# Kernel tuning notes

Hardware: AMD Instinct MI355X
Metric: run time of the kernel (lower is better)

## Reference

```python
import jax, jax.numpy as jnp
import numpy as np

B, N, D_PATCH = 32, 196, 768
TKN, QK, H, HID = 768, 64, 12, 3072
K_STEPS = 12
ALPHA = 1.0
BETA = 1.0 / (QK ** 0.5)
EPS = 1e-5


def setup_inputs() -> dict:
    key = jax.random.key(0)
    ks = jax.random.split(key, 8)
    w_std = 0.002
    return {
        "x": jax.random.normal(ks[0], (B, N, D_PATCH), jnp.float32),
        "w_enc": jax.random.normal(ks[1], (TKN, D_PATCH), jnp.float32) * 0.02,
        "b_enc": jnp.zeros((TKN,), jnp.float32),
        "cls_tok": jnp.ones((1, 1, TKN), jnp.float32),
        "pos": jax.random.normal(ks[2], (1, N + 1, TKN), jnp.float32) * w_std,
        "eln_gamma": jnp.ones((1,), jnp.float32),
        "eln_bias": jnp.zeros((TKN,), jnp.float32),
        "wq": jax.random.normal(ks[3], (H, QK, TKN), jnp.float32) * w_std,
        "wk": jax.random.normal(ks[4], (H, QK, TKN), jnp.float32) * w_std,
        "w_hop": jax.random.normal(ks[5], (HID, TKN), jnp.float32) * 0.02,
        "dec_ln_w": jnp.ones((TKN,), jnp.float32),
        "dec_ln_b": jnp.zeros((TKN,), jnp.float32),
        "w_dec": jax.random.normal(ks[6], (D_PATCH, TKN), jnp.float32) * 0.02,
        "b_dec": jnp.zeros((D_PATCH,), jnp.float32),
    }


def _energy(g, wq, wk, w_hop):
    # attention energy: non-softmax, -1/beta * sum logsumexp(beta * A)
    q = jnp.einsum('bnd,hzd->bnhz', g, wq)
    k = jnp.einsum('bnd,hzd->bnhz', g, wk)
    A = jnp.einsum('bqhz,bkhz->bhqk', q, k)  # [B,H,N+1,N+1]
    e_attn = (-1.0 / BETA) * jnp.sum(jax.nn.logsumexp(BETA * A, axis=-1))
    # Hopfield energy: -0.5 * sum relu(g W^T)^2
    h = jnp.einsum('bnd,fd->bnf', g, w_hop)  # [B,N+1,HID]
    e_hop = -0.5 * jnp.sum(jax.nn.relu(h) ** 2)
    return e_attn + e_hop


def _energy_ln(x, gamma, bias):
    xm = x - x.mean(-1, keepdims=True)
    o = xm / jnp.sqrt((xm ** 2).mean(-1, keepdims=True) + EPS)
    return gamma * o + bias


def _layernorm(x, w, b):
    mu = x.mean(-1, keepdims=True)
    xm = x - mu
    var = (xm ** 2).mean(-1, keepdims=True)
    return xm / jnp.sqrt(var + EPS) * w + b


def reference(x, w_enc, b_enc, cls_tok, pos, eln_gamma, eln_bias,
              wq, wk, w_hop, dec_ln_w, dec_ln_b, w_dec, b_dec):
    # encode: Linear(d_patch -> tkn)
    t = jnp.einsum('bnd,td->bnt', x, w_enc) + b_enc
    # prepend cls, add positional encoding
    cls = jnp.broadcast_to(cls_tok, (t.shape[0], 1, TKN))
    t = jnp.concatenate([cls, t], axis=1) + pos  # [B, N+1, TKN]

    grad_e = jax.grad(lambda g: _energy(g, wq, wk, w_hop))
    for _ in range(K_STEPS):  # fixed unroll over time steps (single block)
        g = _energy_ln(t, eln_gamma, eln_bias)
        t = t - ALPHA * grad_e(g)

    # decode: LayerNorm + Linear(tkn -> d_patch)
    y = _layernorm(t, dec_ln_w, dec_ln_b)
    y = jnp.einsum('bnt,dt->bnd', y, w_dec) + b_dec
    return y[:, 1:]  # drop cls token (use_cls=False)
```

## Files before the change

### kernel.cpp

```cpp
#include <hip/hip_runtime.h>
#include <hip/hip_bf16.h>

typedef __hip_bfloat16 bf16;
typedef short s8 __attribute__((ext_vector_type(8)));
typedef short sv4 __attribute__((ext_vector_type(4)));
typedef float f4 __attribute__((ext_vector_type(4)));

#define BETA 0.125f
#define EPS 1e-5f

__device__ __forceinline__ void gld16(const void* g, void* l){
    __builtin_amdgcn_global_load_lds(
        (const __attribute__((address_space(1))) void*)g,
        (__attribute__((address_space(3))) void*)l, 16, 0, 0);
}

__global__ __launch_bounds__(256) void f2b_k(const float* __restrict__ in, bf16* __restrict__ out, long n){
    long i = (long)blockIdx.x*256 + threadIdx.x;
    if (i < n) out[i] = __float2bfloat16(in[i]);
}
__global__ __launch_bounds__(256) void padx_k(const float* __restrict__ x, bf16* __restrict__ xb){
    long i = (long)blockIdx.x*256 + threadIdx.x;
    if (i >= 6400L*768) return;
    long row = i / 768;
    xb[i] = (row < 6272) ? __float2bfloat16(x[i]) : __float2bfloat16(0.f);
}
__global__ __launch_bounds__(256) void tr_k(const short* __restrict__ Bi, short* __restrict__ Bo){
    __shared__ short t[32][33];
    int i0 = blockIdx.x*32, j0 = blockIdx.y*32;
    int li = threadIdx.x & 31, lj = threadIdx.x >> 5;
    #pragma unroll
    for (int r=0;r<4;r++) t[lj+8*r][li] = Bi[(long)(i0+lj+8*r)*768 + j0+li];
    __syncthreads();
    #pragma unroll
    for (int r=0;r<4;r++) Bo[(long)(j0+lj+8*r)*4608 + i0+li] = t[li][lj+8*r];
}

__global__ __launch_bounds__(256) void cls_k(const float* __restrict__ cls, const float* __restrict__ pos,
                                             float* __restrict__ t){
    int i = blockIdx.x*256 + threadIdx.x;
    int b = i / 768, c = i % 768;
    t[((long)b*197)*768 + c] = cls[c] + pos[c];
}

template<int MODE>
__global__ __launch_bounds__(256) void big_gemm(
    const short* __restrict__ A, int lda,
    const short* __restrict__ B, int ldb,
    float* __restrict__ Cf, bf16* __restrict__ Cb, int ldc,
    int K, int Nn, int Nm, int relu0, long zoff,
    const float* __restrict__ bias, const float* __restrict__ pos)
{
    const int f = blockIdx.x;
    const int npg = 16*Nn;
    const int grp = f / npg;
    const int first_m = grp*16;
    const int gs = (Nm - first_m < 16) ? (Nm - first_m) : 16;
    const int rem = f % npg;
    const int bm = first_m + rem % gs;
    const int bn = rem / gs;

    __shared__ short lsA[8192];
    __shared__ short lsB[8192];
    const int tid = threadIdx.x;
    const int w = tid>>6, l = tid&63;
    const int m0 = bm*128, n0 = bn*128;
    const int srow = tid>>2;
    const int qglob = ((tid&3) - (tid>>3)) & 3;
    const int scol = qglob*8;
    int koff, Ks;
    if (MODE==1){ Ks = K>>1; koff = blockIdx.z * Ks; Cf += (size_t)blockIdx.z * zoff; }
    else        { Ks = K;    koff = 0; }
    const short* pa = A + (size_t)(m0+srow)*lda + koff + scol;
    const short* pb = B + (size_t)(n0+srow)*ldb + koff + scol;
    short* laP = lsA + w*512;
    short* lbP = lsB + w*512;
    const int wm = (w>>1)*64, wn = (w&1)*64;
    const int fr = l&15, fq = ((l>>4) + (fr>>1) & 3)*8;
    f4 acc[4][4] = {};
    const int nk = Ks>>6;
    for (int kt=0; kt<nk; kt++){
        const size_t ko = (size_t)kt*64;
        const size_t ra = 64*(size_t)lda, rb = 64*(size_t)ldb;
        gld16(pa + ko,           laP);
        gld16(pa + ko + ra,      laP + 2048);
        gld16(pa + ko + 32,      laP + 4096);
        gld16(pa + ko + 32 + ra, laP + 6144);
        gld16(pb + ko,           lbP);
        gld16(pb + ko + rb,      lbP + 2048);
        gld16(pb + ko + 32,      lbP + 4096);
        gld16(pb + ko + 32 + rb, lbP + 6144);
        __syncthreads();
        #pragma unroll
        for (int ks=0; ks<2; ks++){
            s8 af[4], bfr[4];
            #pragma unroll
            for (int i=0;i<4;i++) af[i]  = *(const s8*)(lsA + ks*4096 + (wm+i*16+fr)*32 + fq);
            #pragma unroll
            for (int j=0;j<4;j++) bfr[j] = *(const s8*)(lsB + ks*4096 + (wn+j*16+fr)*32 + fq);
            #pragma unroll
            for (int i=0;i<4;i++)
                #pragma unroll
                for (int j=0;j<4;j++)
                    acc[i][j] = __builtin_amdgcn_mfma_f32_16x16x32_bf16(af[i], bfr[j], acc[i][j], 0,0,0);
        }
        __syncthreads();
    }
    const int er = (l>>4)*4;
    const int ec = l&15;
    #pragma unroll
    for (int i=0;i<4;i++){
        #pragma unroll
        for (int j=0;j<4;j++){
            int gr0 = m0 + wm + i*16 + er;
            int gc  = n0 + wn + j*16 + ec;
            #pragma unroll
            for (int r=0;r<4;r++){
                float v = acc[i][j][r];
                int gr = gr0 + r;
                if (MODE==0){
                    if (gc >= relu0) v = v>0.f ? v : 0.f;
                    Cb[(size_t)gr*ldc + gc] = __float2bfloat16(v);
                } else if (MODE==1){
                    Cf[(size_t)gr*ldc + gc] = v;
                } else if (MODE==2){
                    if (gr < 6272){
                        int b = gr/196, n = gr%196;
                        Cf[((size_t)b*197 + n + 1)*768 + gc] = v + bias[gc] + pos[(long)(n+1)*768+gc];
                    }
                } else {
                    if (gr < 6272) Cf[(size_t)gr*ldc + gc] = v + bias[gc];
                }
            }
        }
    }
}

template<int MODE>
__global__ __launch_bounds__(256, 2) void wide_gemm(
    const short* __restrict__ A, int lda,
    const short* __restrict__ B, int ldb,
    float* __restrict__ Cf, float* __restrict__ Cf2,
    bf16* __restrict__ Cb, int ldc,
    int K, int Nn, int Nm, int relu0, long zoff)
{
    const int f = blockIdx.x;
    const int npg = 16*Nn;
    const int grp = f / npg;
    const int first_m = grp*16;
    const int gs = (Nm - first_m < 16) ? (Nm - first_m) : 16;
    const int rem = f % npg;
    const int bm = first_m + rem % gs;
    const int bn = rem / gs;

    __shared__ short lsA[16384];
    __shared__ short lsB[8192];
    const int tid = threadIdx.x;
    const int w = tid>>6, l = tid&63;
    const int m0 = bm*256, n0 = bn*128;

    int Ks, koff; float* Cp = Cf;
    if (MODE==1){ Ks = K/3; koff = blockIdx.z * Ks;
                  Cp = (blockIdx.z==2) ? Cf2 : Cf + (size_t)blockIdx.z * zoff; }
    else        { Ks = K; koff = 0; }
    const int NT = Ks>>6;

    const short* sA[4]; const short* sB[2];
    #pragma unroll
    for (int j=0;j<4;j++){
        int c = j*256 + tid;
        int r = (c>>2)&255, qd = c&3;
        int qs = (qd - (r>>1)) & 3;
        sA[j] = A + (size_t)(m0+r)*lda + koff + qs*8;
    }
    #pragma unroll
    for (int j=0;j<2;j++){
        int c = j*256 + tid;
        int r = (c>>2)&127, qd = c&3;
        int qs = (qd - (r>>1)) & 3;
        sB[j] = B + (size_t)(n0+r)*ldb + koff + qs*8;
    }

    const int wm = (w>>1)*128, wn = (w&1)*64;
    const int fr = l&15;
    const int fq = (((l>>4) + (fr>>1)) & 3)*8;
    f4 acc[8][4] = {};

    for (int kt=0; kt<NT; kt++){
        const size_t ko = (size_t)kt*64;
        short* dA = lsA + w*512;
        short* dB = lsB + w*512;
        #pragma unroll
        for (int j=0;j<4;j++){
            gld16(sA[j]+ko,      dA + j*2048);
            gld16(sA[j]+ko+32,   dA + (j+4)*2048);
        }
        #pragma unroll
        for (int j=0;j<2;j++){
            gld16(sB[j]+ko,      dB + j*2048);
            gld16(sB[j]+ko+32,   dB + (j+2)*2048);
        }
        __syncthreads();
        #pragma unroll
        for (int ks=0; ks<2; ks++){
            s8 af[8], bfr[4];
            #pragma unroll
            for (int i=0;i<8;i++) af[i]  = *(const s8*)(lsA + ks*8192 + (wm+i*16+fr)*32 + fq);
            #pragma unroll
            for (int j=0;j<4;j++) bfr[j] = *(const s8*)(lsB + ks*4096 + (wn+j*16+fr)*32 + fq);
            #pragma unroll
            for (int i=0;i<8;i++)
                #pragma unroll
                for (int j=0;j<4;j++)
                    acc[i][j] = __builtin_amdgcn_mfma_f32_16x16x32_bf16(af[i], bfr[j], acc[i][j], 0,0,0);
        }
        __syncthreads();
    }

    const int er = (l>>4)*4;
    const int ec = l&15;
    #pragma unroll
    for (int i=0;i<8;i++){
        #pragma unroll
        for (int j=0;j<4;j++){
            int gr0 = m0 + wm + i*16 + er;
            int gc  = n0 + wn + j*16 + ec;
            #pragma unroll
            for (int r=0;r<4;r++){
                float v = acc[i][j][r];
                int gr = gr0 + r;
                if (MODE==0){
                    if (gc >= relu0) v = v>0.f ? v : 0.f;
                    Cb[(size_t)gr*ldc + gc] = __float2bfloat16(v);
                } else {
                    Cp[(size_t)gr*ldc + gc] = v;
                }
            }
        }
    }
}

__global__ __launch_bounds__(256) void pack_k(const short* __restrict__ qkh,
                                              short* __restrict__ qT, short* __restrict__ kT){
    __shared__ short tq[64][65];
    __shared__ short tk[64][65];
    const int bh = blockIdx.x, b = bh/12, h = bh%12;
    const int mc = blockIdx.y*64;
    const int tid = threadIdx.x;
    #pragma unroll
    for (int e=0;e<16;e++){
        int i = tid + e*256; int r = i>>6, c = i&63;
        int mg = mc + r;
        short vq = 0, vk = 0;
        if (mg < 197){
            size_t base = (size_t)(b*197+mg)*4608 + h*64 + c;
            vq = qkh[base]; vk = qkh[base+768];
        }
        tq[r][c] = vq; tk[r][c] = vk;
    }
    __syncthreads();
    #pragma unroll
    for (int e=0;e<16;e++){
        int i = tid + e*256; int zr = i>>6, cm = i&63;
        size_t o = (size_t)bh*16384 + (size_t)zr*256 + mc + cm;
        qT[o] = tq[cm][zr];
        kT[o] = tk[cm][zr];
    }
}

__global__ __launch_bounds__(256) void attn_k(
    short* __restrict__ qkh, const short* __restrict__ qT, const short* __restrict__ kT)
{
    __shared__ short Pl[64*232];
    __shared__ short Ptl[208*72];
    const int bh = blockIdx.x, b = bh/12, h = bh%12;
    const int tid = threadIdx.x, w = tid>>6, l = tid&63;
    const int lr = l&15, lq = l>>4;
    const size_t qcol = (size_t)h*64, kcol = 768 + qcol;
    const size_t rbase = (size_t)b*197*4608;
    const short* qTp = qT + (size_t)bh*16384;
    const short* kTp = kT + (size_t)bh*16384;

    for (int i=tid; i<64*16; i+=256){ int r=i>>4, c=208+(i&15); Pl[r*232+c]=0; }

    f4 ak[13];
    #pragma unroll
    for (int t=0;t<13;t++) ak[t] = (f4){0.f,0.f,0.f,0.f};

    for (int iter=0; iter<4; iter++){
        const int m0 = iter*64;
        f4 S[13];
        #pragma unroll
        for (int t=0;t<13;t++) S[t] = (f4){0.f,0.f,0.f,0.f};
        const int mrow = m0 + w*16 + lr;
        #pragma unroll
        for (int ks=0; ks<2; ks++){
            s8 af = *(const s8*)(qkh + rbase + (size_t)mrow*4608 + qcol + ks*32 + lq*8);
            #pragma unroll
            for (int t=0;t<13;t++){
                s8 bf = *(const s8*)(qkh + rbase + (size_t)(t*16+lr)*4608 + kcol + ks*32 + lq*8);
                S[t] = __builtin_amdgcn_mfma_f32_16x16x32_bf16(af, bf, S[t], 0,0,0);
            }
        }
        __syncthreads();
        const int mbase = w*16 + lq*4;
        #pragma unroll
        for (int r=0;r<4;r++){
            float mx = -1e30f;
            #pragma unroll
            for (int t=0;t<13;t++){
                float v = S[t][r]*BETA;
                if (t==12 && lr>=5) v = -1e30f;
                S[t][r] = v;
                mx = fmaxf(mx, v);
            }
            mx = fmaxf(mx, __shfl_xor(mx,1,64)); mx = fmaxf(mx, __shfl_xor(mx,2,64));
            mx = fmaxf(mx, __shfl_xor(mx,4,64)); mx = fmaxf(mx, __shfl_xor(mx,8,64));
            float sm = 0.f;
            #pragma unroll
            for (int t=0;t<13;t++){ float e = __expf(S[t][r]-mx); S[t][r]=e; sm+=e; }
            sm += __shfl_xor(sm,1,64); sm += __shfl_xor(sm,2,64);
            sm += __shfl_xor(sm,4,64); sm += __shfl_xor(sm,8,64);
            float inv = 1.f/sm;
            bool valid = (m0 + mbase + r) < 197;
            #pragma unroll
            for (int t=0;t<13;t++) S[t][r] = valid ? S[t][r]*inv : 0.f;
        }
        #pragma unroll
        for (int t=0;t<13;t++){
            int c = t*16 + lr;
            short pb[4];
            #pragma unroll
            for (int r=0;r<4;r++){
                bf16 bv = __float2bfloat16(S[t][r]);
                pb[r] = *(short*)&bv;
                Pl[(mbase+r)*232 + c] = pb[r];
            }
            *(sv4*)(Ptl + c*72 + mbase) = (sv4){pb[0],pb[1],pb[2],pb[3]};
        }
        __syncthreads();
        f4 aq[4];
        #pragma unroll
        for (int t=0;t<4;t++) aq[t] = (f4){0.f,0.f,0.f,0.f};
        #pragma unroll
        for (int ks=0; ks<7; ks++){
            s8 af = *(const s8*)(kTp + (w*16+lr)*256 + ks*32 + lq*8);
            #pragma unroll
            for (int mt=0;mt<4;mt++){
                s8 bf = *(const s8*)(Pl + (mt*16+lr)*232 + ks*32 + lq*8);
                aq[mt] = __builtin_amdgcn_mfma_f32_16x16x32_bf16(af, bf, aq[mt], 0,0,0);
            }
        }
        #pragma unroll
        for (int mt=0;mt<4;mt++){
            int mg = m0 + mt*16 + lr;
            if (mg < 197){
                sv4 pv;
                #pragma unroll
                for (int r=0;r<4;r++){ bf16 bv=__float2bfloat16(aq[mt][r]); pv[r]=*(short*)&bv; }
                *(sv4*)(qkh + rbase + (size_t)mg*4608 + qcol + w*16 + lq*4) = pv;
            }
        }
        #pragma unroll
        for (int ks=0; ks<2; ks++){
            s8 bf = *(const s8*)(qTp + (w*16+lr)*256 + m0 + ks*32 + lq*8);
            #pragma unroll
            for (int t=0;t<13;t++){
                s8 af = *(const s8*)(Ptl + (t*16+lr)*72 + ks*32 + lq*8);
                ak[t] = __builtin_amdgcn_mfma_f32_16x16x32_bf16(af, bf, ak[t], 0,0,0);
            }
        }
    }
    #pragma unroll
    for (int t=0;t<13;t++){
        #pragma unroll
        for (int r=0;r<4;r++){
            int n = t*16 + lq*4 + r;
            if (n < 197)
                *(bf16*)(qkh + rbase + (size_t)n*4608 + kcol + w*16 + lr) = __float2bfloat16(ak[t][r]);
        }
    }
}

__global__ __launch_bounds__(256) void ln_k(
    float* __restrict__ in, bf16* __restrict__ out,
    const float* __restrict__ p0, const float* __restrict__ p1, const float* __restrict__ p2,
    const float* __restrict__ scale, const float* __restrict__ bias,
    int scalar_scale, int rowmap, int addp, int writet)
{
    int r = blockIdx.x;
    long src = rowmap ? ((long)(r/196)*197 + r%196 + 1) : (long)r;
    float* xr = in + src*768;
    int tid = threadIdx.x;
    float v0 = xr[tid], v1 = xr[tid+256], v2 = xr[tid+512];
    if (addp){
        const float* a = p0 + src*768;
        const float* b = p1 + src*768;
        const float* c = p2 + src*768;
        v0 += a[tid]     + b[tid]     + c[tid];
        v1 += a[tid+256] + b[tid+256] + c[tid+256];
        v2 += a[tid+512] + b[tid+512] + c[tid+512];
        if (writet){ xr[tid]=v0; xr[tid+256]=v1; xr[tid+512]=v2; }
    }
    __shared__ float red[4];
    float s = v0+v1+v2;
    #pragma unroll
    for (int o=1;o<64;o<<=1) s += __shfl_xor(s, o, 64);
    if ((tid&63)==0) red[tid>>6] = s;
    __syncthreads();
    float mu = (red[0]+red[1]+red[2]+red[3]) * (1.f/768.f);
    float d0=v0-mu, d1=v1-mu, d2=v2-mu;
    float q = d0*d0 + d1*d1 + d2*d2;
    #pragma unroll
    for (int o=1;o<64;o<<=1) q += __shfl_xor(q, o, 64);
    __syncthreads();
    if ((tid&63)==0) red[tid>>6] = q;
    __syncthreads();
    float ms = (red[0]+red[1]+red[2]+red[3]) * (1.f/768.f);
    float inv = rsqrtf(ms + EPS);
    bf16* o_ = out + (long)r*768;
    float s0 = scalar_scale ? scale[0] : scale[tid];
    float s1 = scalar_scale ? s0 : scale[tid+256];
    float s2 = scalar_scale ? s0 : scale[tid+512];
    o_[tid]     = __float2bfloat16(d0*inv*s0 + bias[tid]);
    o_[tid+256] = __float2bfloat16(d1*inv*s1 + bias[tid+256]);
    o_[tid+512] = __float2bfloat16(d2*inv*s2 + bias[tid+512]);
}

extern "C" void kernel_launch(void* const* d_in, const int* in_sizes, int n_in,
                              void* d_out, int out_size, void* d_ws, size_t ws_size,
                              hipStream_t stream) {
    const float* x       = (const float*)d_in[0];
    const float* w_enc   = (const float*)d_in[1];
    const float* b_enc   = (const float*)d_in[2];
    const float* cls_tok = (const float*)d_in[3];
    const float* pos     = (const float*)d_in[4];
    const float* eln_g   = (const float*)d_in[5];
    const float* eln_b   = (const float*)d_in[6];
    const float* wq      = (const float*)d_in[7];
    const float* wk      = (const float*)d_in[8];
    const float* w_hop   = (const float*)d_in[9];
    const float* dln_w   = (const float*)d_in[10];
    const float* dln_b   = (const float*)d_in[11];
    const float* w_dec   = (const float*)d_in[12];
    const float* b_dec   = (const float*)d_in[13];
    float* out = (float*)d_out;

    float* t_  = (float*)d_ws;
    bf16* g_   = (bf16*)(t_ + 6400L*768);
    bf16* qkh  = g_ + 6400L*768;
    bf16* qT   = qkh + 6400L*4608;
    bf16* kT   = qT + 384L*16384;
    float* p0  = (float*)(kT + 384L*16384);
    float* p1  = p0 + 6400L*768;
    bf16* B1   = (bf16*)(p1 + 6400L*768);
    bf16* B2   = B1 + 4608L*768;
    bf16* we_  = B2 + 768L*4608;
    bf16* wd_  = we_ + 768L*768;
    float* p2  = (float*)qT;

    dim3 blk(256);
    const long ZOFF = 6400L*768;

    f2b_k<<<dim3((589824+255)/256),  blk, 0, stream>>>(wq,    B1,          589824);
    f2b_k<<<dim3((589824+255)/256),  blk, 0, stream>>>(wk,    B1+589824,   589824);
    f2b_k<<<dim3((2359296+255)/256), blk, 0, stream>>>(w_hop, B1+1179648, 2359296);
    f2b_k<<<dim3((589824+255)/256),  blk, 0, stream>>>(w_enc, we_,         589824);
    f2b_k<<<dim3((589824+255)/256),  blk, 0, stream>>>(w_dec, wd_,         589824);
    tr_k<<<dim3(144,24), blk, 0, stream>>>((const short*)B1, (short*)B2);
    padx_k<<<dim3((int)((6400L*768+255)/256)), blk, 0, stream>>>(x, g_);

    cls_k<<<dim3(96), blk, 0, stream>>>(cls_tok, pos, t_);
    big_gemm<2><<<dim3(300), blk, 0, stream>>>((const short*)g_, 768, (const short*)we_, 768,
                                               t_, nullptr, 768, 768, 6, 50, 0, 0, b_enc, pos);

    for (int step=0; step<12; step++){
        ln_k<<<dim3(6304), blk, 0, stream>>>(t_, g_, p0, p1, p2, eln_g, eln_b, 1, 0, step>0, 1);
        wide_gemm<0><<<dim3(900), blk, 0, stream>>>((const short*)g_, 768, (const short*)B1, 768,
                                                    nullptr, nullptr, qkh, 4608, 768, 36, 25, 1536, 0);
        pack_k<<<dim3(384,4), blk, 0, stream>>>((const short*)qkh, (short*)qT, (short*)kT);
        attn_k<<<dim3(384), blk, 0, stream>>>((short*)qkh, (const short*)qT, (const short*)kT);
        wide_gemm<1><<<dim3(150,1,3), blk, 0, stream>>>((const short*)qkh, 4608, (const short*)B2, 4608,
                                                        p0, p2, nullptr, 768, 4608, 6, 25, 0, ZOFF);
    }

    ln_k<<<dim3(6272), blk, 0, stream>>>(t_, g_, p0, p1, p2, dln_w, dln_b, 0, 1, 1, 0);
    big_gemm<3><<<dim3(300), blk, 0, stream>>>((const short*)g_, 768, (const short*)wd_, 768,
                                               out, nullptr, 768, 768, 6, 50, 0, 0, b_dec, nullptr);
}
```

Before: 2.448 ms.

## Double-buffer GEMM LDS tiles with BK=32 to overlap loads and MFMA

Changes the GEMM main loop from single-buffered 64-wide K tiles with two barriers per step to double-buffered 32-wide K tiles. The next tile's global-to-LDS loads are issued before computing on the current buffer, so memory latency can overlap with MFMA work, and only one barrier is needed per step. It also raises wave priority around the MFMA block. In exchange it doubles the number of iterations, halves the work per barrier, and may hit LDS hazards if the direct-to-LDS loads are not waited on before the barrier.

```diff
diff --git a/kernel.cpp b/kernel.cpp
--- a/kernel.cpp
+++ b/kernel.cpp
@@ -163,20 +163,20 @@
     if (MODE==1){ Ks = K/3; koff = blockIdx.z * Ks;
                   Cp = (blockIdx.z==2) ? Cf2 : Cf + (size_t)blockIdx.z * zoff; }
     else        { Ks = K; koff = 0; }
-    const int NT = Ks>>6;
+    const int NT = Ks>>5;
 
     const short* sA[4]; const short* sB[2];
     #pragma unroll
     for (int j=0;j<4;j++){
         int c = j*256 + tid;
-        int r = (c>>2)&255, qd = c&3;
+        int r = c>>2, qd = c&3;
         int qs = (qd - (r>>1)) & 3;
         sA[j] = A + (size_t)(m0+r)*lda + koff + qs*8;
     }
     #pragma unroll
     for (int j=0;j<2;j++){
         int c = j*256 + tid;
-        int r = (c>>2)&127, qd = c&3;
+        int r = c>>2, qd = c&3;
         int qs = (qd - (r>>1)) & 3;
         sB[j] = B + (size_t)(n0+r)*ldb + koff + qs*8;
     }
@@ -186,35 +186,43 @@
     const int fq = (((l>>4) + (fr>>1)) & 3)*8;
     f4 acc[8][4] = {};
 
-    for (int kt=0; kt<NT; kt++){
-        const size_t ko = (size_t)kt*64;
-        short* dA = lsA + w*512;
-        short* dB = lsB + w*512;
-        #pragma unroll
-        for (int j=0;j<4;j++){
-            gld16(sA[j]+ko,      dA + j*2048);
-            gld16(sA[j]+ko+32,   dA + (j+4)*2048);
-        }
-        #pragma unroll
-        for (int j=0;j<2;j++){
-            gld16(sB[j]+ko,      dB + j*2048);
-            gld16(sB[j]+ko+32,   dB + (j+2)*2048);
-        }
+    short* dA0 = lsA + w*512;
+    short* dB0 = lsB + w*512;
+
+    #pragma unroll
+    for (int j=0;j<4;j++) gld16(sA[j], dA0 + j*2048);
+    #pragma unroll
+    for (int j=0;j<2;j++) gld16(sB[j], dB0 + j*2048);
+    __syncthreads();
+
+    int buf = 0;
+    for (int t=0; t<NT; t++){
+        if (t+1 < NT){
+            const size_t ko = (size_t)(t+1)*32;
+            short* dA = dA0 + (buf^1)*8192;
+            short* dB = dB0 + (buf^1)*4096;
+            #pragma unroll
+            for (int j=0;j<4;j++) gld16(sA[j]+ko, dA + j*2048);
+            #pragma unroll
+            for (int j=0;j<2;j++) gld16(sB[j]+ko, dB + j*2048);
+        }
+        __builtin_amdgcn_sched_barrier(0);
+        const short* aP = lsA + buf*8192;
+        const short* bP = lsB + buf*4096;
+        s8 af[8], bfr[4];
+        #pragma unroll
+        for (int i=0;i<8;i++) af[i]  = *(const s8*)(aP + (wm+i*16+fr)*32 + fq);
+        #pragma unroll
+        for (int j=0;j<4;j++) bfr[j] = *(const s8*)(bP + (wn+j*16+fr)*32 + fq);
+        __builtin_amdgcn_s_setprio(1);
+        #pragma unroll
+        for (int i=0;i<8;i++)
+            #pragma unroll
+            for (int j=0;j<4;j++)
+                acc[i][j] = __builtin_amdgcn_mfma_f32_16x16x32_bf16(af[i], bfr[j], acc[i][j], 0,0,0);
+        __builtin_amdgcn_s_setprio(0);
         __syncthreads();
-        #pragma unroll
-        for (int ks=0; ks<2; ks++){
-            s8 af[8], bfr[4];
-            #pragma unroll
-            for (int i=0;i<8;i++) af[i]  = *(const s8*)(lsA + ks*8192 + (wm+i*16+fr)*32 + fq);
-            #pragma unroll
-            for (int j=0;j<4;j++) bfr[j] = *(const s8*)(lsB + ks*4096 + (wn+j*16+fr)*32 + fq);
-            #pragma unroll
-            for (int i=0;i<8;i++)
-                #pragma unroll
-                for (int j=0;j<4;j++)
-                    acc[i][j] = __builtin_amdgcn_mfma_f32_16x16x32_bf16(af[i], bfr[j], acc[i][j], 0,0,0);
-        }
-        __syncthreads();
+        buf ^= 1;
     }
 
     const int er = (l>>4)*4;
```

Result: slower. 2.586 ms (+5.6%).

## Replace wide GEMM with 512-thread 256x256 double-buffered pipelined kernel

Applied to the files above, without the earlier changes.

Swaps the 256-thread 256x128-tile GEMM used for the QK/Hopfield projection and the gradient back-projection for an 8-wave kernel with 256x256 tiles. LDS is double-buffered, with the next k-tile's global-to-LDS loads interleaved between MFMA sub-phases, and s_setprio/sched_barrier shape the schedule. The aim is to hide global load latency and raise arithmetic intensity per tile. In exchange it uses 128KB of LDS per block, which limits occupancy to one block per CU, and launches half as many blocks (450 and 75x3), which risks poorer CU utilisation on tail waves.

```diff
diff --git a/kernel.cpp b/kernel.cpp
--- a/kernel.cpp
+++ b/kernel.cpp
@@ -137,7 +137,7 @@
 }
 
 template<int MODE>
-__global__ __launch_bounds__(256, 2) void wide_gemm(
+__global__ __launch_bounds__(512) void gem8(
     const short* __restrict__ A, int lda,
     const short* __restrict__ B, int ldb,
     float* __restrict__ Cf, float* __restrict__ Cf2,
@@ -153,11 +153,11 @@
     const int bm = first_m + rem % gs;
     const int bn = rem / gs;
 
-    __shared__ short lsA[16384];
-    __shared__ short lsB[8192];
+    __shared__ short lsA[32768];
+    __shared__ short lsB[32768];
     const int tid = threadIdx.x;
     const int w = tid>>6, l = tid&63;
-    const int m0 = bm*256, n0 = bn*128;
+    const int m0 = bm*256, n0 = bn*256;
 
     int Ks, koff; float* Cp = Cf;
     if (MODE==1){ Ks = K/3; koff = blockIdx.z * Ks;
@@ -165,59 +165,91 @@
     else        { Ks = K; koff = 0; }
     const int NT = Ks>>6;
 
-    const short* sA[4]; const short* sB[2];
-    #pragma unroll
-    for (int j=0;j<4;j++){
-        int c = j*256 + tid;
-        int r = (c>>2)&255, qd = c&3;
-        int qs = (qd - (r>>1)) & 3;
-        sA[j] = A + (size_t)(m0+r)*lda + koff + qs*8;
-    }
-    #pragma unroll
-    for (int j=0;j<2;j++){
-        int c = j*256 + tid;
-        int r = (c>>2)&127, qd = c&3;
-        int qs = (qd - (r>>1)) & 3;
-        sB[j] = B + (size_t)(n0+r)*ldb + koff + qs*8;
-    }
-
-    const int wm = (w>>1)*128, wn = (w&1)*64;
-    const int fr = l&15;
-    const int fq = (((l>>4) + (fr>>1)) & 3)*8;
+    const int srow = tid>>2;
+    const int qs = ((tid&3) - (tid>>3)) & 3;
+    const short* pa = A + (size_t)(m0+srow)*lda + koff + qs*8;
+    const short* pb = B + (size_t)(n0+srow)*ldb + koff + qs*8;
+    const int wds = w*512;
+
+    #define STA(S,H,KS,KT) gld16(pa + (size_t)(H)*128*lda + (size_t)(KT)*64 + (KS)*32, \
+                                 lsA + (S)*16384 + (H)*8192 + (KS)*4096 + wds)
+    #define STB(S,H,KS,KT) gld16(pb + (size_t)(H)*128*ldb + (size_t)(KT)*64 + (KS)*32, \
+                                 lsB + (S)*16384 + (H)*8192 + (KS)*4096 + wds)
+
+    const int wm = (w>>2)*128, wn = (w&3)*64;
+    const int hA = wm>>7;
+    const int hB = wn>>7;
+    const int wnl = wn & 64;
+    const int fr = l&15, lq = l>>4;
+    const int fq = ((lq + (fr>>1)) & 3)*8;
     f4 acc[8][4] = {};
 
+    STA(0,0,0,0); STA(0,0,1,0); STA(0,1,0,0); STA(0,1,1,0);
+    STB(0,0,0,0); STB(0,0,1,0); STB(0,1,0,0); STB(0,1,1,0);
+    __syncthreads();
+
+    int s = 0;
     for (int kt=0; kt<NT; kt++){
-        const size_t ko = (size_t)kt*64;
-        short* dA = lsA + w*512;
-        short* dB = lsB + w*512;
-        #pragma unroll
-        for (int j=0;j<4;j++){
-            gld16(sA[j]+ko,      dA + j*2048);
-            gld16(sA[j]+ko+32,   dA + (j+4)*2048);
-        }
-        #pragma unroll
-        for (int j=0;j<2;j++){
-            gld16(sB[j]+ko,      dB + j*2048);
-            gld16(sB[j]+ko+32,   dB + (j+2)*2048);
-        }
+        const int nx = (kt+1 < NT);
+        const short* aB = lsA + s*16384 + hA*8192;
+        const short* bB = lsB + s*16384 + hB*8192;
+        s8 af[4], bfr[4];
+        if (nx){ STA(s^1,0,0,kt+1); STA(s^1,0,1,kt+1); STA(s^1,1,0,kt+1); STA(s^1,1,1,kt+1); }
+        __builtin_amdgcn_sched_barrier(0);
+        #pragma unroll
+        for (int i=0;i<4;i++) af[i]  = *(const s8*)(aB + (i*16+fr)*32 + fq);
+        #pragma unroll
+        for (int j=0;j<4;j++) bfr[j] = *(const s8*)(bB + (wnl+j*16+fr)*32 + fq);
+        __builtin_amdgcn_s_setprio(1);
+        #pragma unroll
+        for (int i=0;i<4;i++)
+            #pragma unroll
+            for (int j=0;j<4;j++)
+                acc[i][j] = __builtin_amdgcn_mfma_f32_16x16x32_bf16(af[i], bfr[j], acc[i][j], 0,0,0);
+        __builtin_amdgcn_s_setprio(0);
+        __builtin_amdgcn_s_barrier();
+        if (nx){ STB(s^1,0,0,kt+1); STB(s^1,0,1,kt+1); }
+        __builtin_amdgcn_sched_barrier(0);
+        #pragma unroll
+        for (int i=0;i<4;i++) af[i] = *(const s8*)(aB + ((64+i*16)+fr)*32 + fq);
+        __builtin_amdgcn_s_setprio(1);
+        #pragma unroll
+        for (int i=0;i<4;i++)
+            #pragma unroll
+            for (int j=0;j<4;j++)
+                acc[4+i][j] = __builtin_amdgcn_mfma_f32_16x16x32_bf16(af[i], bfr[j], acc[4+i][j], 0,0,0);
+        __builtin_amdgcn_s_setprio(0);
+        __builtin_amdgcn_s_barrier();
+        if (nx){ STB(s^1,1,0,kt+1); STB(s^1,1,1,kt+1); }
+        __builtin_amdgcn_sched_barrier(0);
+        #pragma unroll
+        for (int i=0;i<4;i++) af[i]  = *(const s8*)(aB + 4096 + (i*16+fr)*32 + fq);
+        #pragma unroll
+        for (int j=0;j<4;j++) bfr[j] = *(const s8*)(bB + 4096 + (wnl+j*16+fr)*32 + fq);
+        __builtin_amdgcn_s_setprio(1);
+        #pragma unroll
+        for (int i=0;i<4;i++)
+            #pragma unroll
+            for (int j=0;j<4;j++)
+                acc[i][j] = __builtin_amdgcn_mfma_f32_16x16x32_bf16(af[i], bfr[j], acc[i][j], 0,0,0);
+        __builtin_amdgcn_s_setprio(0);
+        __builtin_amdgcn_s_barrier();
+        #pragma unroll
+        for (int i=0;i<4;i++) af[i] = *(const s8*)(aB + 4096 + ((64+i*16)+fr)*32 + fq);
+        __builtin_amdgcn_s_setprio(1);
+        #pragma unroll
+        for (int i=0;i<4;i++)
+            #pragma unroll
+            for (int j=0;j<4;j++)
+                acc[4+i][j] = __builtin_amdgcn_mfma_f32_16x16x32_bf16(af[i], bfr[j], acc[4+i][j], 0,0,0);
+        __builtin_amdgcn_s_setprio(0);
         __syncthreads();
-        #pragma unroll
-        for (int ks=0; ks<2; ks++){
-            s8 af[8], bfr[4];
-            #pragma unroll
-            for (int i=0;i<8;i++) af[i]  = *(const s8*)(lsA + ks*8192 + (wm+i*16+fr)*32 + fq);
-            #pragma unroll
-            for (int j=0;j<4;j++) bfr[j] = *(const s8*)(lsB + ks*4096 + (wn+j*16+fr)*32 + fq);
-            #pragma unroll
-            for (int i=0;i<8;i++)
-                #pragma unroll
-                for (int j=0;j<4;j++)
-                    acc[i][j] = __builtin_amdgcn_mfma_f32_16x16x32_bf16(af[i], bfr[j], acc[i][j], 0,0,0);
-        }
-        __syncthreads();
-    }
-
-    const int er = (l>>4)*4;
+        s ^= 1;
+    }
+    #undef STA
+    #undef STB
+
+    const int er = lq*4;
     const int ec = l&15;
     #pragma unroll
     for (int i=0;i<8;i++){
@@ -476,12 +508,12 @@
 
     for (int step=0; step<12; step++){
         ln_k<<<dim3(6304), blk, 0, stream>>>(t_, g_, p0, p1, p2, eln_g, eln_b, 1, 0, step>0, 1);
-        wide_gemm<0><<<dim3(900), blk, 0, stream>>>((const short*)g_, 768, (const short*)B1, 768,
-                                                    nullptr, nullptr, qkh, 4608, 768, 36, 25, 1536, 0);
+        gem8<0><<<dim3(450), dim3(512), 0, stream>>>((const short*)g_, 768, (const short*)B1, 768,
+                                                     nullptr, nullptr, qkh, 4608, 768, 18, 25, 1536, 0);
         pack_k<<<dim3(384,4), blk, 0, stream>>>((const short*)qkh, (short*)qT, (short*)kT);
         attn_k<<<dim3(384), blk, 0, stream>>>((short*)qkh, (const short*)qT, (const short*)kT);
-        wide_gemm<1><<<dim3(150,1,3), blk, 0, stream>>>((const short*)qkh, 4608, (const short*)B2, 4608,
-                                                        p0, p2, nullptr, 768, 4608, 6, 25, 0, ZOFF);
+        gem8<1><<<dim3(75,1,3), dim3(512), 0, stream>>>((const short*)qkh, 4608, (const short*)B2, 4608,
+                                                        p0, p2, nullptr, 768, 4608, 3, 25, 0, ZOFF);
     }
 
     ln_k<<<dim3(6272), blk, 0, stream>>>(t_, g_, p0, p1, p2, dln_w, dln_b, 0, 1, 1, 0);
```

Measured after the change: 2.910 ms. +18.9%, slower.
